# Kernel optimization log

Hardware: AMD Instinct MI355X
Metric: run time of the kernel (lower is better)

Reference implementation:

```python
import jax, jax.numpy as jnp
import numpy as np

SEQ, B, IN, H, GATES = 2048, 64, 64, 128, 4 * 128


def setup_inputs() -> dict:
    key = jax.random.key(0)
    ks = jax.random.split(key, 12)
    s_in = 1.0 / np.sqrt(H)
    return {
        "data": jax.random.normal(ks[0], (SEQ, B, IN), dtype=jnp.float32),
        "Wih0": jax.random.normal(ks[1], (GATES, IN), dtype=jnp.float32) * s_in,
        "Whh0": jax.random.normal(ks[2], (GATES, H), dtype=jnp.float32) * s_in,
        "bih0": jax.random.normal(ks[3], (GATES,), dtype=jnp.float32) * s_in,
        "bhh0": jax.random.normal(ks[4], (GATES,), dtype=jnp.float32) * s_in,
        "Wih1": jax.random.normal(ks[5], (GATES, H), dtype=jnp.float32) * s_in,
        "Whh1": jax.random.normal(ks[6], (GATES, H), dtype=jnp.float32) * s_in,
        "bih1": jax.random.normal(ks[7], (GATES,), dtype=jnp.float32) * s_in,
        "bhh1": jax.random.normal(ks[8], (GATES,), dtype=jnp.float32) * s_in,
        "Wlin": jax.random.normal(ks[9], (1, H), dtype=jnp.float32) * s_in,
        "blin": jax.random.normal(ks[10], (1,), dtype=jnp.float32) * s_in,
    }


def _lstm_layer(x, Wih, Whh, bih, bhh):
    # x: [T, B, D_in]; torch gate order: i, f, g, o
    Bsz = x.shape[1]
    Hd = Whh.shape[1]
    b = bih + bhh
    # Precompute input projections for all timesteps in one big GEMM: [T, B, 4H]
    xproj = jnp.einsum('tbd,gd->tbg', x, Wih) + b

    def step(carry, xp_t):
        h, c = carry
        gates = xp_t + h @ Whh.T  # [B, 4H]
        i, f, g, o = jnp.split(gates, 4, axis=-1)
        i = jax.nn.sigmoid(i)
        f = jax.nn.sigmoid(f)
        g = jnp.tanh(g)
        o = jax.nn.sigmoid(o)
        c = f * c + i * g
        h = o * jnp.tanh(c)
        return (h, c), h

    h0 = jnp.zeros((Bsz, Hd), x.dtype)
    (_, _), ys = jax.lax.scan(step, (h0, h0), xproj)
    return ys  # [T, B, H]


def reference(data, Wih0, Whh0, bih0, bhh0, Wih1, Whh1, bih1, bhh1, Wlin, blin):
    h = _lstm_layer(data, Wih0, Whh0, bih0, bhh0)
    h = _lstm_layer(h, Wih1, Whh1, bih1, bhh1)
    vecs = h @ Wlin.T + blin  # [T, B, 1]
    # NOTE: original module computes tanh(vecs) but returns the pre-tanh vecs.
    return vecs
```

## Files before the change

### kernel.cpp

```cpp
#include <hip/hip_runtime.h>

#define SEQ_T 2048
#define BATCH 64

typedef _Float16 half2v __attribute__((ext_vector_type(2)));

#if defined(__has_builtin)
#  if __has_builtin(__builtin_amdgcn_fdot2)
#    define HAVE_FDOT2 1
#  endif
#endif

__device__ __forceinline__ float fdot2f(half2v a, half2v b, float c) {
#ifdef HAVE_FDOT2
  return __builtin_amdgcn_fdot2(a, b, c, false);
#else
  return c + (float)a[0] * (float)b[0] + (float)a[1] * (float)b[1];
#endif
}

__device__ __forceinline__ unsigned int h2u(half2v v) { return __builtin_bit_cast(unsigned int, v); }
__device__ __forceinline__ half2v u2h(unsigned int u) { return __builtin_bit_cast(half2v, u); }

__device__ __forceinline__ float sigmoid_fast(float x) {
  return 1.f / (1.f + __expf(-x));
}
__device__ __forceinline__ float tanh_fast(float x) {
  return 1.f - 2.f / (1.f + __expf(2.f * x));
}

template <int K, bool IN_F32>
__global__ __launch_bounds__(512) void xproj_gemm(
    const void* __restrict__ Xv,
    const float* __restrict__ W,
    const float* __restrict__ bih, const float* __restrict__ bhh,
    unsigned short* __restrict__ xp)
{
  constexpr int MT = 64;
  const int g = threadIdx.x;
  const size_t m0 = (size_t)blockIdx.x * MT;

  __shared__ __align__(16) _Float16 xs[MT * K];

  if constexpr (IN_F32) {
    constexpr int PER = MT * K / 512;
    const float* Xf = (const float*)Xv + m0 * K + (size_t)g * PER;
    _Float16* dst = xs + g * PER;
#pragma unroll
    for (int i = 0; i < PER; i += 4) {
      float4 v = *reinterpret_cast<const float4*>(Xf + i);
      half2v h01; h01[0] = (_Float16)v.x; h01[1] = (_Float16)v.y;
      half2v h23; h23[0] = (_Float16)v.z; h23[1] = (_Float16)v.w;
      uint2 u; u.x = h2u(h01); u.y = h2u(h23);
      *reinterpret_cast<uint2*>(dst + i) = u;
    }
  } else {
    constexpr int PER = MT * K / 512;
    const unsigned short* Xh = (const unsigned short*)Xv + m0 * K + (size_t)g * PER;
#pragma unroll
    for (int i = 0; i < PER / 8; i++)
      reinterpret_cast<uint4*>(xs + g * PER)[i] = reinterpret_cast<const uint4*>(Xh)[i];
  }

  half2v wr[K / 2];
  {
    const float2* p = reinterpret_cast<const float2*>(W + (size_t)g * K);
#pragma unroll
    for (int k = 0; k < K / 2; k++) {
      float2 f = p[k];
      half2v v; v[0] = (_Float16)f.x; v[1] = (_Float16)f.y;
      wr[k] = v;
    }
  }
  const float bias = bih[g] + bhh[g];
  const int out_off = (g & 127) * 4 + (g >> 7);
  __syncthreads();

#pragma unroll 1
  for (int tb = 0; tb < MT; tb++) {
    const uint4* xv = reinterpret_cast<const uint4*>(xs + tb * K);
    float a0 = bias, a1 = 0.f, a2 = 0.f, a3 = 0.f;
#pragma unroll
    for (int i = 0; i < K / 8; i++) {
      const uint4 u = xv[i];
      a0 = fdot2f(wr[4 * i + 0], u2h(u.x), a0);
      a1 = fdot2f(wr[4 * i + 1], u2h(u.y), a1);
      a2 = fdot2f(wr[4 * i + 2], u2h(u.z), a2);
      a3 = fdot2f(wr[4 * i + 3], u2h(u.w), a3);
    }
    const float s = (a0 + a1) + (a2 + a3);
    xp[(m0 + tb) * 512 + out_off] = __builtin_bit_cast(unsigned short, (_Float16)s);
  }
}

__device__ __forceinline__ void lstm_step(
    int t, int cur, int ks, int r, int b,
    const half2v (&wh)[4][16], _Float16 (&hbuf)[2][128],
    unsigned short& pf, const unsigned short* __restrict__ xpb,
    float& c, unsigned short* __restrict__ hout)
{
  const float xpv = (float)__builtin_bit_cast(_Float16, pf);
  const int tn = (t + 2 < SEQ_T) ? (t + 2) : (SEQ_T - 1);
  pf = xpb[(size_t)tn * (BATCH * 512)];

  float a0 = (ks == 0) ? xpv : 0.f;
  float a1 = (ks == 1) ? xpv : 0.f;
  float a2 = (ks == 2) ? xpv : 0.f;
  float a3 = (ks == 3) ? xpv : 0.f;

  const uint4* hv = reinterpret_cast<const uint4*>(&hbuf[cur][0]);
#pragma unroll
  for (int i = 0; i < 4; i++) {
    const uint4 u = hv[ks * 4 + i];
    a0 = fdot2f(wh[0][4 * i + 0], u2h(u.x), a0);
    a0 = fdot2f(wh[0][4 * i + 1], u2h(u.y), a0);
    a0 = fdot2f(wh[0][4 * i + 2], u2h(u.z), a0);
    a0 = fdot2f(wh[0][4 * i + 3], u2h(u.w), a0);
    a1 = fdot2f(wh[1][4 * i + 0], u2h(u.x), a1);
    a1 = fdot2f(wh[1][4 * i + 1], u2h(u.y), a1);
    a1 = fdot2f(wh[1][4 * i + 2], u2h(u.z), a1);
    a1 = fdot2f(wh[1][4 * i + 3], u2h(u.w), a1);
    a2 = fdot2f(wh[2][4 * i + 0], u2h(u.x), a2);
    a2 = fdot2f(wh[2][4 * i + 1], u2h(u.y), a2);
    a2 = fdot2f(wh[2][4 * i + 2], u2h(u.z), a2);
    a2 = fdot2f(wh[2][4 * i + 3], u2h(u.w), a2);
    a3 = fdot2f(wh[3][4 * i + 0], u2h(u.x), a3);
    a3 = fdot2f(wh[3][4 * i + 1], u2h(u.y), a3);
    a3 = fdot2f(wh[3][4 * i + 2], u2h(u.z), a3);
    a3 = fdot2f(wh[3][4 * i + 3], u2h(u.w), a3);
  }

  a0 += __shfl_xor(a0, 1); a0 += __shfl_xor(a0, 2);
  a1 += __shfl_xor(a1, 1); a1 += __shfl_xor(a1, 2);
  a2 += __shfl_xor(a2, 1); a2 += __shfl_xor(a2, 2);
  a3 += __shfl_xor(a3, 1); a3 += __shfl_xor(a3, 2);

  const float gi = sigmoid_fast(a0);
  const float gf = sigmoid_fast(a1);
  const float gg = tanh_fast(a2);
  const float go = sigmoid_fast(a3);
  c = gf * c + gi * gg;
  const float h = go * tanh_fast(c);

  if (ks == 0) {
    hbuf[cur ^ 1][r] = (_Float16)h;
    hout[((size_t)t * BATCH + b) * 128 + r] =
        __builtin_bit_cast(unsigned short, (_Float16)h);
  }
  asm volatile("s_waitcnt lgkmcnt(0)" ::: "memory");
  __builtin_amdgcn_s_barrier();
}

__global__ __launch_bounds__(512, 2) void lstm_rec2(
    const float* __restrict__ Whh,
    const unsigned short* __restrict__ xp,
    unsigned short* __restrict__ hout)
{
  const int b = blockIdx.x;
  const int tid = threadIdx.x;
  const int l = tid & 63;
  const int w = tid >> 6;
  const int rr = l >> 2;
  const int ks = l & 3;
  const int r = w * 16 + rr;

  __shared__ __align__(16) _Float16 hbuf[2][128];

  half2v wh[4][16];
#pragma unroll
  for (int g = 0; g < 4; g++) {
    const float2* p = reinterpret_cast<const float2*>(
        Whh + ((size_t)(g * 128 + r)) * 128 + ks * 32);
#pragma unroll
    for (int k = 0; k < 16; k++) {
      float2 f = p[k];
      half2v v; v[0] = (_Float16)f.x; v[1] = (_Float16)f.y;
      wh[g][k] = v;
    }
  }

  if (tid < 128) hbuf[0][tid] = (_Float16)0.f;

  const unsigned short* xpb = xp + (size_t)b * 512 + tid;
  unsigned short pfa = xpb[0];
  unsigned short pfb = xpb[(size_t)1 * (BATCH * 512)];
  float c = 0.f;
  __syncthreads();

#pragma unroll 1
  for (int t = 0; t < SEQ_T; t += 2) {
    lstm_step(t,     0, ks, r, b, wh, hbuf, pfa, xpb, c, hout);
    lstm_step(t + 1, 1, ks, r, b, wh, hbuf, pfb, xpb, c, hout);
  }
}

__global__ __launch_bounds__(256) void final_lin(
    const unsigned short* __restrict__ h1,
    const float* __restrict__ Wlin, const float* __restrict__ blin,
    float* __restrict__ out)
{
  const size_t tb = (size_t)blockIdx.x * 256 + threadIdx.x;
  half2v wl[64];
  const float2* p = reinterpret_cast<const float2*>(Wlin);
#pragma unroll
  for (int k = 0; k < 64; k++) {
    float2 f = p[k];
    half2v v; v[0] = (_Float16)f.x; v[1] = (_Float16)f.y;
    wl[k] = v;
  }
  const uint4* hv = reinterpret_cast<const uint4*>(h1 + tb * 128);
  float a0 = 0.f, a1 = 0.f, a2 = 0.f, a3 = 0.f;
#pragma unroll
  for (int i = 0; i < 16; i++) {
    const uint4 u = hv[i];
    a0 = fdot2f(wl[4 * i + 0], u2h(u.x), a0);
    a1 = fdot2f(wl[4 * i + 1], u2h(u.y), a1);
    a2 = fdot2f(wl[4 * i + 2], u2h(u.z), a2);
    a3 = fdot2f(wl[4 * i + 3], u2h(u.w), a3);
  }
  out[tb] = (a0 + a1) + (a2 + a3) + blin[0];
}

extern "C" void kernel_launch(void* const* d_in, const int* in_sizes, int n_in,
                              void* d_out, int out_size, void* d_ws, size_t ws_size,
                              hipStream_t stream) {
  (void)in_sizes; (void)n_in; (void)out_size; (void)ws_size;

  const float* data = (const float*)d_in[0];
  const float* Wih0 = (const float*)d_in[1];
  const float* Whh0 = (const float*)d_in[2];
  const float* bih0 = (const float*)d_in[3];
  const float* bhh0 = (const float*)d_in[4];
  const float* Wih1 = (const float*)d_in[5];
  const float* Whh1 = (const float*)d_in[6];
  const float* bih1 = (const float*)d_in[7];
  const float* bhh1 = (const float*)d_in[8];
  const float* Wlin = (const float*)d_in[9];
  const float* blin = (const float*)d_in[10];

  unsigned char* ws = (unsigned char*)d_ws;
  unsigned short* xpb = (unsigned short*)ws;
  unsigned short* h0 = (unsigned short*)(ws + (size_t)128 * 1024 * 1024);
  unsigned short* h1 = (unsigned short*)(ws + (size_t)160 * 1024 * 1024);

  const int M = SEQ_T * BATCH;
  const int gemm_blocks = M / 64;

  xproj_gemm<64, true><<<dim3(gemm_blocks), dim3(512), 0, stream>>>(
      data, Wih0, bih0, bhh0, xpb);
  lstm_rec2<<<dim3(BATCH), dim3(512), 0, stream>>>(Whh0, xpb, h0);
  xproj_gemm<128, false><<<dim3(gemm_blocks), dim3(512), 0, stream>>>(
      h0, Wih1, bih1, bhh1, xpb);
  lstm_rec2<<<dim3(BATCH), dim3(512), 0, stream>>>(Whh1, xpb, h1);
  final_lin<<<dim3(M / 256), dim3(256), 0, stream>>>(h1, Wlin, blin, (float*)d_out);
}
```

Baseline: 3.399 ms.

## Switch recurrent LSTM step to fp32 packed FMA with lane-distributed gate activations

The recurrent kernel now keeps W_hh and the hidden-state buffer in fp32 and uses packed fp32 FMAs in place of fp16 dot2. The LDS buffer is padded to reduce bank conflicts. Partial sums are combined with a transpose-style shuffle reduction so each lane ends up owning one gate and evaluates a single sigmoid (tanh is expressed through a scaled sigmoid). The four gates are then gathered by shuffles. Prefetch and output addressing move to incrementing pointers, and the manual waitcnt+barrier is replaced with __syncthreads. The fp32 weights double register use per thread, which risks spilling under the 512x2 launch bound.

After: 3.195 ms. 6.0% less time.

```diff
diff --git a/kernel.cpp b/kernel.cpp
--- a/kernel.cpp
+++ b/kernel.cpp
@@ -4,6 +4,7 @@
 #define BATCH 64
 
 typedef _Float16 half2v __attribute__((ext_vector_type(2)));
+typedef float floatx2 __attribute__((ext_vector_type(2)));
 
 #if defined(__has_builtin)
 #  if __has_builtin(__builtin_amdgcn_fdot2)
@@ -19,15 +20,19 @@
 #endif
 }
 
+__device__ __forceinline__ floatx2 fma2(floatx2 a, floatx2 b, floatx2 c) {
+#if __has_builtin(__builtin_elementwise_fma)
+  return __builtin_elementwise_fma(a, b, c);
+#else
+  floatx2 r;
+  r.x = __builtin_fmaf(a.x, b.x, c.x);
+  r.y = __builtin_fmaf(a.y, b.y, c.y);
+  return r;
+#endif
+}
+
 __device__ __forceinline__ unsigned int h2u(half2v v) { return __builtin_bit_cast(unsigned int, v); }
 __device__ __forceinline__ half2v u2h(unsigned int u) { return __builtin_bit_cast(half2v, u); }
-
-__device__ __forceinline__ float sigmoid_fast(float x) {
-  return 1.f / (1.f + __expf(-x));
-}
-__device__ __forceinline__ float tanh_fast(float x) {
-  return 1.f - 2.f / (1.f + __expf(2.f * x));
-}
 
 template <int K, bool IN_F32>
 __global__ __launch_bounds__(512) void xproj_gemm(
@@ -93,62 +98,73 @@
   }
 }
 
+struct StepCtx {
+  int ks, r, hidx;
+  int li0, li1, li2, li3;
+  float sc, am, ab;
+  bool writer;
+};
+
+__device__ __forceinline__ float sigmoid_fast(float x) {
+  return 1.f / (1.f + __expf(-x));
+}
+
 __device__ __forceinline__ void lstm_step(
-    int t, int cur, int ks, int r, int b,
-    const half2v (&wh)[4][16], _Float16 (&hbuf)[2][128],
-    unsigned short& pf, const unsigned short* __restrict__ xpb,
-    float& c, unsigned short* __restrict__ hout)
+    int cur, const StepCtx& cx,
+    const floatx2 (&wh)[4][16], float (&hbuf)[2][144],
+    unsigned short& pf, const unsigned short*& pf_ptr,
+    float& c, unsigned short*& hout_ptr)
 {
   const float xpv = (float)__builtin_bit_cast(_Float16, pf);
-  const int tn = (t + 2 < SEQ_T) ? (t + 2) : (SEQ_T - 1);
-  pf = xpb[(size_t)tn * (BATCH * 512)];
-
-  float a0 = (ks == 0) ? xpv : 0.f;
-  float a1 = (ks == 1) ? xpv : 0.f;
-  float a2 = (ks == 2) ? xpv : 0.f;
-  float a3 = (ks == 3) ? xpv : 0.f;
-
-  const uint4* hv = reinterpret_cast<const uint4*>(&hbuf[cur][0]);
-#pragma unroll
-  for (int i = 0; i < 4; i++) {
-    const uint4 u = hv[ks * 4 + i];
-    a0 = fdot2f(wh[0][4 * i + 0], u2h(u.x), a0);
-    a0 = fdot2f(wh[0][4 * i + 1], u2h(u.y), a0);
-    a0 = fdot2f(wh[0][4 * i + 2], u2h(u.z), a0);
-    a0 = fdot2f(wh[0][4 * i + 3], u2h(u.w), a0);
-    a1 = fdot2f(wh[1][4 * i + 0], u2h(u.x), a1);
-    a1 = fdot2f(wh[1][4 * i + 1], u2h(u.y), a1);
-    a1 = fdot2f(wh[1][4 * i + 2], u2h(u.z), a1);
-    a1 = fdot2f(wh[1][4 * i + 3], u2h(u.w), a1);
-    a2 = fdot2f(wh[2][4 * i + 0], u2h(u.x), a2);
-    a2 = fdot2f(wh[2][4 * i + 1], u2h(u.y), a2);
-    a2 = fdot2f(wh[2][4 * i + 2], u2h(u.z), a2);
-    a2 = fdot2f(wh[2][4 * i + 3], u2h(u.w), a2);
-    a3 = fdot2f(wh[3][4 * i + 0], u2h(u.x), a3);
-    a3 = fdot2f(wh[3][4 * i + 1], u2h(u.y), a3);
-    a3 = fdot2f(wh[3][4 * i + 2], u2h(u.z), a3);
-    a3 = fdot2f(wh[3][4 * i + 3], u2h(u.w), a3);
-  }
-
-  a0 += __shfl_xor(a0, 1); a0 += __shfl_xor(a0, 2);
-  a1 += __shfl_xor(a1, 1); a1 += __shfl_xor(a1, 2);
-  a2 += __shfl_xor(a2, 1); a2 += __shfl_xor(a2, 2);
-  a3 += __shfl_xor(a3, 1); a3 += __shfl_xor(a3, 2);
-
-  const float gi = sigmoid_fast(a0);
-  const float gf = sigmoid_fast(a1);
-  const float gg = tanh_fast(a2);
-  const float go = sigmoid_fast(a3);
+  pf = *pf_ptr;
+  pf_ptr += 2 * BATCH * 512;
+
+  floatx2 a0 = {0.f, 0.f}, a1 = {0.f, 0.f}, a2 = {0.f, 0.f}, a3 = {0.f, 0.f};
+  const float4* hv = reinterpret_cast<const float4*>(&hbuf[cur][cx.ks * 36]);
+#pragma unroll
+  for (int i = 0; i < 8; i++) {
+    const float4 u = hv[i];
+    floatx2 lo; lo.x = u.x; lo.y = u.y;
+    floatx2 hi; hi.x = u.z; hi.y = u.w;
+    a0 = fma2(wh[0][2 * i], lo, a0); a0 = fma2(wh[0][2 * i + 1], hi, a0);
+    a1 = fma2(wh[1][2 * i], lo, a1); a1 = fma2(wh[1][2 * i + 1], hi, a1);
+    a2 = fma2(wh[2][2 * i], lo, a2); a2 = fma2(wh[2][2 * i + 1], hi, a2);
+    a3 = fma2(wh[3][2 * i], lo, a3); a3 = fma2(wh[3][2 * i + 1], hi, a3);
+  }
+  float b0v = a0.x + a0.y;
+  float b1v = a1.x + a1.y;
+  float b2v = a2.x + a2.y;
+  float b3v = a3.x + a3.y;
+
+  const bool q0 = (cx.ks & 1) != 0, q1 = (cx.ks & 2) != 0;
+  float s0 = q0 ? b0v : b1v;
+  float s1 = q0 ? b2v : b3v;
+  float r0 = __shfl_xor(s0, 1);
+  float r1 = __shfl_xor(s1, 1);
+  float kA = (q0 ? b1v : b0v) + r0;
+  float kB = (q0 ? b3v : b2v) + r1;
+  float s2 = q1 ? kA : kB;
+  float r2 = __shfl_xor(s2, 2);
+  float sum = (q1 ? kB : kA) + r2 + xpv;
+
+  float y = cx.am * sigmoid_fast(cx.sc * sum) + cx.ab;
+
+  float gi = __shfl(y, cx.li0);
+  float gf = __shfl(y, cx.li1);
+  float gg = __shfl(y, cx.li2);
+  float go = __shfl(y, cx.li3);
+
   c = gf * c + gi * gg;
-  const float h = go * tanh_fast(c);
-
-  if (ks == 0) {
-    hbuf[cur ^ 1][r] = (_Float16)h;
-    hout[((size_t)t * BATCH + b) * 128 + r] =
-        __builtin_bit_cast(unsigned short, (_Float16)h);
-  }
-  asm volatile("s_waitcnt lgkmcnt(0)" ::: "memory");
-  __builtin_amdgcn_s_barrier();
+  float th = 2.f * sigmoid_fast(2.f * c) - 1.f;
+  float h = go * th;
+
+  if (cx.writer) {
+    hbuf[cur ^ 1][cx.hidx] = h;
+    *hout_ptr = __builtin_bit_cast(unsigned short, (_Float16)h);
+  }
+  hout_ptr += BATCH * 128;
+
+  __syncthreads();
 }
 
 __global__ __launch_bounds__(512, 2) void lstm_rec2(
@@ -164,33 +180,48 @@
   const int ks = l & 3;
   const int r = w * 16 + rr;
 
-  __shared__ __align__(16) _Float16 hbuf[2][128];
-
-  half2v wh[4][16];
+  __shared__ __align__(16) float hbuf[2][144];
+
+  floatx2 wh[4][16];
 #pragma unroll
   for (int g = 0; g < 4; g++) {
-    const float2* p = reinterpret_cast<const float2*>(
+    const float4* p = reinterpret_cast<const float4*>(
         Whh + ((size_t)(g * 128 + r)) * 128 + ks * 32);
 #pragma unroll
-    for (int k = 0; k < 16; k++) {
-      float2 f = p[k];
-      half2v v; v[0] = (_Float16)f.x; v[1] = (_Float16)f.y;
-      wh[g][k] = v;
-    }
-  }
-
-  if (tid < 128) hbuf[0][tid] = (_Float16)0.f;
+    for (int k = 0; k < 8; k++) {
+      float4 f = p[k];
+      floatx2 lo; lo.x = f.x; lo.y = f.y;
+      floatx2 hi; hi.x = f.z; hi.y = f.w;
+      wh[g][2 * k] = lo;
+      wh[g][2 * k + 1] = hi;
+    }
+  }
+
+  StepCtx cx;
+  cx.ks = ks; cx.r = r;
+  cx.hidx = (r >> 5) * 36 + (r & 31);
+  const int lb = l & ~3;
+  cx.li0 = lb + 0; cx.li1 = lb + 1; cx.li2 = lb + 2; cx.li3 = lb + 3;
+  cx.sc = (ks == 2) ? 2.f : 1.f;
+  cx.am = (ks == 2) ? 2.f : 1.f;
+  cx.ab = (ks == 2) ? -1.f : 0.f;
+  cx.writer = (ks == 0);
+
+  if (tid < 144) { hbuf[0][tid] = 0.f; }
 
   const unsigned short* xpb = xp + (size_t)b * 512 + tid;
   unsigned short pfa = xpb[0];
   unsigned short pfb = xpb[(size_t)1 * (BATCH * 512)];
+  const unsigned short* pA = xpb + (size_t)2 * (BATCH * 512);
+  const unsigned short* pB = xpb + (size_t)3 * (BATCH * 512);
+  unsigned short* houtp = hout + (size_t)b * 128 + r;
   float c = 0.f;
   __syncthreads();
 
 #pragma unroll 1
   for (int t = 0; t < SEQ_T; t += 2) {
-    lstm_step(t,     0, ks, r, b, wh, hbuf, pfa, xpb, c, hout);
-    lstm_step(t + 1, 1, ks, r, b, wh, hbuf, pfb, xpb, c, hout);
+    lstm_step(0, cx, wh, hbuf, pfa, pA, c, houtp);
+    lstm_step(1, cx, wh, hbuf, pfb, pB, c, houtp);
   }
 }
 
```
